# Optimization experiments

Measured on AMD Instinct MI355X. Metric: run time of the kernel, lower is better.

The kernel has to match this reference:

```python
import jax, jax.numpy as jnp
import numpy as np

H = 4096      # hidden_size
NH = 32       # num_heads
QR = 1536     # q_lora_rank
KVR = 512     # kv_lora_rank
RD = 64       # qk_rope_head_dim
ND = 128      # qk_nope_head_dim
VD = 128      # v_head_dim
QK = RD + ND  # qk_head_dim
EPS = 1e-6
THETA = 10000.0
B, S = 2, 1024


def rmsnorm(x, w):
    # torch: x / (||x|| * d^-0.5 + eps) * w
    norm = jnp.sqrt(jnp.sum(x * x, axis=-1, keepdims=True)) * (x.shape[-1] ** -0.5)
    return x / (norm + EPS) * w


def rope_cos_sin(seq_len):
    inv_freq = 1.0 / (THETA ** (jnp.arange(0, RD, 2, dtype=jnp.float32) / RD))
    t = jnp.arange(seq_len, dtype=jnp.float32)
    freqs = jnp.outer(t, inv_freq)              # [S, RD/2]
    emb = jnp.concatenate([freqs, freqs], -1)   # [S, RD]
    return jnp.cos(emb), jnpp_cos_sin_dummy() if False else jnp.sin(emb)


def rotate_half(x):
    x1, x2 = jnp.split(x, 2, axis=-1)
    return jnp.concatenate([-x2, x1], axis=-1)


def setup_inputs() -> dict:
    key = jax.random.key(0)
    ks = jax.random.split(key, 8)
    sc = 0.02
    return {
        "hidden_states": jax.random.normal(ks[0], (B, S, H), jnp.float32),
        "w_qa": jax.random.normal(ks[1], (H, QR), jnp.float32) * sc,
        "g_qa": jnp.ones((QR,), jnp.float32),
        "w_qb": jax.random.normal(ks[2], (QR, NH * QK), jnp.float32) * sc,
        "w_kva": jax.random.normal(ks[3], (H, KVR + RD), jnp.float32) * sc,
        "g_kva": jnp.ones((KVR,), jnp.float32),
        "w_kvb": jax.random.normal(ks[4], (KVR, NH * (ND + VD)), jnp.float32) * sc,
        "w_o": jax.random.normal(ks[5], (NH * VD, H), jnp.float32) * sc,
    }


def reference(hidden_states, w_qa, g_qa, w_qb, w_kva, g_kva, w_kvb, w_o):
    b, s, _ = hidden_states.shape
    # Q path: LoRA down -> RMSNorm -> LoRA up
    q_c = rmsnorm(hidden_states @ w_qa, g_qa)                       # [b,s,QR]
    q = (q_c @ w_qb).reshape(b, s, NH, QK).transpose(0, 2, 1, 3)    # [b,NH,s,QK]
    q_nope, q_rope = q[..., :ND], q[..., ND:]
    # KV path: joint down-proj, split compressed kv and rope key
    kv = hidden_states @ w_kva                                      # [b,s,KVR+RD]
    k_c, k_rope = kv[..., :KVR], kv[..., KVR:]
    k_c = rmsnorm(k_c, g_kva)
    kst = (k_c @ w_kvb).reshape(b, s, NH, ND + VD).transpose(0, 2, 1, 3)
    k_nope, v = kst[..., :ND], kst[..., ND:]                        # [b,NH,s,ND],[b,NH,s,VD]
    # partial RoPE on the rope slice only
    inv_freq = 1.0 / (THETA ** (jnp.arange(0, RD, 2, dtype=jnp.float32) / RD))
    freqs = jnp.outer(jnp.arange(s, dtype=jnp.float32), inv_freq)
    emb = jnp.concatenate([freqs, freqs], -1)                       # [s,RD]
    cos = jnp.cos(emb)[None, None]                                  # [1,1,s,RD]
    sin = jnp.sin(emb)[None, None]
    k_rope = k_rope[:, None]                                        # [b,1,s,RD]
    q_rope = q_rope * cos + rotate_half(q_rope) * sin
    k_rope = k_rope * cos + rotate_half(k_rope) * sin
    k_rope = jnp.broadcast_to(k_rope, (b, NH, s, RD))
    query = jnp.concatenate([q_nope, q_rope], -1)                   # [b,NH,s,QK]
    key_s = jnp.concatenate([k_nope, k_rope], -1)
    scaling = QK ** -0.5
    scores = jnp.einsum("bhqd,bhkd->bhqk", query, key_s) * scaling  # [b,NH,s,s]
    attn = jax.nn.softmax(scores, axis=-1)
    out = jnp.einsum("bhqk,bhkd->bhqd", attn, v)                    # [b,NH,s,VD]
    out = out.transpose(0, 2, 1, 3).reshape(b, s, NH * VD)
    return out @ w_o                                                # [b,s,H]
```

## Files before the change

### kernel.cpp

```cpp
#include <hip/hip_runtime.h>
#include <hip/hip_bf16.h>
#include <stdint.h>

typedef float f32x4_t __attribute__((ext_vector_type(4)));
typedef short s16x8_t __attribute__((ext_vector_type(8)));

#define LDS_AS __attribute__((address_space(3)))
#define GLB_AS __attribute__((address_space(1)))

__device__ __forceinline__ void gload16(void* lds, const void* g) {
    __builtin_amdgcn_global_load_lds((const GLB_AS uint32_t*)g,
                                     (LDS_AS uint32_t*)lds, 16, 0, 0);
}

__global__ __launch_bounds__(256) void rope_table_kernel(float* __restrict__ cos_t,
                                                         float* __restrict__ sin_t) {
    int idx = blockIdx.x * 256 + threadIdx.x;
    int s = idx >> 6, j = idx & 63;
    float invf = powf(10000.0f, -((float)((j & 31) * 2)) / 64.0f);
    float a = (float)s * invf;
    cos_t[idx] = cosf(a);
    sin_t[idx] = sinf(a);
}

__global__ __launch_bounds__(256) void f32_to_bf16_kernel(const float* __restrict__ in,
                                                          __hip_bfloat16* __restrict__ out, int n4) {
    int i = blockIdx.x * 256 + threadIdx.x;
    if (i >= n4) return;
    float4 v = reinterpret_cast<const float4*>(in)[i];
    struct __align__(8) BF4 { __hip_bfloat16 a, b, c, d; } r;
    r.a = __float2bfloat16(v.x); r.b = __float2bfloat16(v.y);
    r.c = __float2bfloat16(v.z); r.d = __float2bfloat16(v.w);
    reinterpret_cast<BF4*>(out)[i] = r;
}

__global__ __launch_bounds__(256) void transpose_convert(const float* __restrict__ W,
                                                         __hip_bfloat16* __restrict__ WT,
                                                         int K, int N, int Npad) {
    __shared__ float tile[32][33];
    int k0 = blockIdx.y * 32, n0 = blockIdx.x * 32;
    int tx = threadIdx.x & 31, ty = threadIdx.x >> 5;
#pragma unroll
    for (int i = 0; i < 4; i++) {
        int ky = i * 8 + ty;
        int n = n0 + tx;
        float v = 0.f;
        if (n < N) v = W[(size_t)(k0 + ky) * N + n];
        tile[ky][tx] = v;
    }
    __syncthreads();
#pragma unroll
    for (int i = 0; i < 4; i++) {
        int ny = i * 8 + ty;
        WT[(size_t)(n0 + ny) * K + k0 + tx] = __float2bfloat16(tile[tx][ny]);
    }
}

__global__ __launch_bounds__(256) void rmsnorm_kernel(const float* __restrict__ in,
                                                      const float* __restrict__ g,
                                                      __hip_bfloat16* __restrict__ out,
                                                      int cols, int in_stride) {
    int row = blockIdx.x;
    const float* x = in + (size_t)row * in_stride;
    float ss = 0.f;
    for (int c = threadIdx.x; c < cols; c += 256) { float v = x[c]; ss += v * v; }
#pragma unroll
    for (int off = 32; off > 0; off >>= 1) ss += __shfl_xor(ss, off);
    __shared__ float red[4];
    if ((threadIdx.x & 63) == 0) red[threadIdx.x >> 6] = ss;
    __syncthreads();
    float tot = red[0] + red[1] + red[2] + red[3];
    float rms = sqrtf(tot / (float)cols);
    float inv = 1.0f / (rms + 1e-6f);
    for (int c = threadIdx.x; c < cols; c += 256)
        out[(size_t)row * cols + c] = __float2bfloat16(x[c] * inv * g[c]);
}

__global__ __launch_bounds__(256) void rope_k_kernel(const float* __restrict__ kv,
                                                     const float* __restrict__ cos_t,
                                                     const float* __restrict__ sin_t,
                                                     __hip_bfloat16* __restrict__ k_rope) {
    int idx = blockIdx.x * 256 + threadIdx.x;
    int tok = idx >> 5, j = idx & 31;
    int s = tok & 1023;
    const float* x = kv + (size_t)tok * 640 + 512;
    float x1 = x[j], x2 = x[j + 32];
    float co = cos_t[s * 64 + j], si = sin_t[s * 64 + j];
    __hip_bfloat16* o = k_rope + (size_t)tok * 64;
    o[j]      = __float2bfloat16(x1 * co - x2 * si);
    o[j + 32] = __float2bfloat16(x2 * co + x1 * si);
}

__global__ __launch_bounds__(256) void rope_scale_q_kernel(__hip_bfloat16* __restrict__ q,
                                                           const float* __restrict__ cos_t,
                                                           const float* __restrict__ sin_t) {
    int tok = blockIdx.x;
    int s = tok & 1023;
    __hip_bfloat16* row = q + (size_t)tok * 6144;
    const float scale = 0.07216878364870323f;
    for (int i = threadIdx.x; i < 4096; i += 256) {
        int h = i >> 7, d = i & 127;
        int c = h * 192 + d;
        row[c] = __float2bfloat16(__bfloat162float(row[c]) * scale);
    }
    for (int i = threadIdx.x; i < 1024; i += 256) {
        int h = i >> 5, j = i & 31;
        int c = h * 192 + 128 + j;
        float x1 = __bfloat162float(row[c]), x2 = __bfloat162float(row[c + 32]);
        float co = cos_t[s * 64 + j], si = sin_t[s * 64 + j];
        row[c]      = __float2bfloat16((x1 * co - x2 * si) * scale);
        row[c + 32] = __float2bfloat16((x2 * co + x1 * si) * scale);
    }
}

__global__ __launch_bounds__(256) void transpose_v_kernel(const __hip_bfloat16* __restrict__ kst,
                                                          __hip_bfloat16* __restrict__ V_T) {
    __shared__ __hip_bfloat16 t[64][136];
    int bid = blockIdx.x;
    int st = bid & 15, bh = bid >> 4;
    int h = bh & 31, b = bh >> 5;
    int s0 = st * 64;
#pragma unroll
    for (int i = 0; i < 4; i++) {
        int c = i * 256 + threadIdx.x;
        int r = c >> 4, oct = c & 15;
        *(s16x8_t*)&t[r][oct * 8] =
            *(const s16x8_t*)&kst[(size_t)(b * 1024 + s0 + r) * 8192 + h * 256 + 128 + oct * 8];
    }
    __syncthreads();
#pragma unroll
    for (int i = 0; i < 4; i++) {
        int c = i * 256 + threadIdx.x;
        int vd = c >> 3, oct = c & 7;
        s16x8_t pk;
#pragma unroll
        for (int e = 0; e < 8; e++) pk[e] = *(const short*)&t[oct * 8 + e][vd];
        *(s16x8_t*)&V_T[((size_t)bh * 128 + vd) * 1024 + s0 + oct * 8] = pk;
    }
}

template <int OUT_BF16>
__global__ __launch_bounds__(256, 2) void gemm_bt_128(const __hip_bfloat16* __restrict__ A,
                                                      const __hip_bfloat16* __restrict__ BT,
                                                      void* __restrict__ Cout,
                                                      int M, int N, int K) {
    __shared__ __hip_bfloat16 As[128 * 64];
    __shared__ __hip_bfloat16 Bs[128 * 64];
    const int tid = threadIdx.x;
    const int l = tid & 63, w = tid >> 6;
    const int wr = w >> 1, wc = w & 1;
    const int m0 = blockIdx.y * 128, n0 = blockIdx.x * 128;
    const int lrow = l & 15, lkg = l >> 4;

    f32x4_t acc[4][4];
#pragma unroll
    for (int i = 0; i < 4; i++)
#pragma unroll
        for (int j = 0; j < 4; j++) acc[i][j] = (f32x4_t){0.f, 0.f, 0.f, 0.f};

    for (int k0 = 0; k0 < K; k0 += 64) {
        __syncthreads();
#pragma unroll
        for (int i = 0; i < 4; i++) {
            int s = i * 256 + tid;
            int row = s >> 3, po = s & 7;
            int lo = po ^ (row & 7);
            gload16(&As[s * 8], &A[(size_t)(m0 + row) * K + k0 + lo * 8]);
            gload16(&Bs[s * 8], &BT[(size_t)(n0 + row) * K + k0 + lo * 8]);
        }
        __syncthreads();
#pragma unroll
        for (int ks = 0; ks < 2; ks++) {
            s16x8_t a[4], b[4];
#pragma unroll
            for (int m = 0; m < 4; m++) {
                int row = wr * 64 + m * 16 + lrow;
                int oct = (ks * 4 + lkg) ^ (row & 7);
                a[m] = *(const s16x8_t*)&As[row * 64 + oct * 8];
            }
#pragma unroll
            for (int n = 0; n < 4; n++) {
                int row = wc * 64 + n * 16 + lrow;
                int oct = (ks * 4 + lkg) ^ (row & 7);
                b[n] = *(const s16x8_t*)&Bs[row * 64 + oct * 8];
            }
#pragma unroll
            for (int m = 0; m < 4; m++)
#pragma unroll
                for (int n = 0; n < 4; n++)
                    acc[m][n] = __builtin_amdgcn_mfma_f32_16x16x32_bf16(a[m], b[n], acc[m][n], 0, 0, 0);
        }
    }
#pragma unroll
    for (int m = 0; m < 4; m++) {
        int row = m0 + wr * 64 + m * 16 + lkg * 4;
#pragma unroll
        for (int n = 0; n < 4; n++) {
            int col = n0 + wc * 64 + n * 16 + lrow;
#pragma unroll
            for (int r = 0; r < 4; r++) {
                float v = acc[m][n][r];
                if (OUT_BF16)
                    ((__hip_bfloat16*)Cout)[(size_t)(row + r) * N + col] = __float2bfloat16(v);
                else
                    ((float*)Cout)[(size_t)(row + r) * N + col] = v;
            }
        }
    }
}

__global__ __launch_bounds__(256, 2) void attn2_kernel(const __hip_bfloat16* __restrict__ q,
                                                       const __hip_bfloat16* __restrict__ kst,
                                                       const __hip_bfloat16* __restrict__ k_rope,
                                                       const __hip_bfloat16* __restrict__ V_T,
                                                       __hip_bfloat16* __restrict__ attn_out) {
    __shared__ __align__(16) __hip_bfloat16 Ks[2][64 * 192];
    __shared__ __align__(16) __hip_bfloat16 Ps[64 * 72];

    int i = blockIdx.x;
    int bh = (i & 7) * 8 + ((i >> 3) & 7);
    int qt = i >> 6;
    int h = bh & 31, b = bh >> 5;
    int q0 = qt * 64;
    int tid = threadIdx.x, l = tid & 63, w = tid >> 6;
    int lrow = l & 15, lkg = l >> 4;

    s16x8_t qa[6];
    {
        size_t qbase = (size_t)(b * 1024 + q0 + w * 16 + lrow) * 6144 + h * 192;
#pragma unroll
        for (int f = 0; f < 6; f++)
            qa[f] = *(const s16x8_t*)&q[qbase + f * 32 + lkg * 8];
    }
    f32x4_t acc_o[8];
#pragma unroll
    for (int n = 0; n < 8; n++) acc_o[n] = (f32x4_t){0.f, 0.f, 0.f, 0.f};
    float m_run[4] = {-1e30f, -1e30f, -1e30f, -1e30f};
    float l_run[4] = {0.f, 0.f, 0.f, 0.f};

    size_t krow_base = (size_t)(b * 1024) * 8192 + h * 256;
    size_t rrow_base = (size_t)(b * 1024) * 64;

    auto stage_k = [&](int kv0, int buf) {
#pragma unroll
        for (int it = 0; it < 6; it++) {
            int s = it * 256 + tid;
            int row = s / 24, po = s - row * 24;
            int lo = po ^ (row & 7);
            const __hip_bfloat16* src = (lo < 16)
                ? &kst[krow_base + (size_t)(kv0 + row) * 8192 + lo * 8]
                : &k_rope[rrow_base + (size_t)(kv0 + row) * 64 + (lo - 16) * 8];
            gload16(&Ks[buf][s * 8], src);
        }
    };

    stage_k(0, 0);
    asm volatile("s_waitcnt vmcnt(0)" ::: "memory");
    __syncthreads();

    int cur = 0;
    for (int kt = 0; kt < 16; kt++) {
        int kv0 = kt * 64;
        if (kt < 15) stage_k(kv0 + 64, cur ^ 1);

        f32x4_t sc[4];
#pragma unroll
        for (int c = 0; c < 4; c++) sc[c] = (f32x4_t){0.f, 0.f, 0.f, 0.f};
        __builtin_amdgcn_s_setprio(1);
#pragma unroll
        for (int c = 0; c < 4; c++) {
            int row = c * 16 + lrow;
#pragma unroll
            for (int f = 0; f < 6; f++) {
                int po = ((f * 4 + lkg) ^ (lrow & 7)) * 8;
                s16x8_t kb = *(const s16x8_t*)&Ks[cur][row * 192 + po];
                sc[c] = __builtin_amdgcn_mfma_f32_16x16x32_bf16(qa[f], kb, sc[c], 0, 0, 0);
            }
        }
        __builtin_amdgcn_s_setprio(0);

        s16x8_t vb[2][8];
#pragma unroll
        for (int kk = 0; kk < 2; kk++)
#pragma unroll
            for (int n = 0; n < 8; n++)
                vb[kk][n] = *(const s16x8_t*)&V_T[((size_t)(bh * 128 + n * 16 + lrow)) * 1024 +
                                                  kv0 + kk * 32 + lkg * 8];

        float mx[4];
#pragma unroll
        for (int r = 0; r < 4; r++) {
            float m0 = fmaxf(fmaxf(sc[0][r], sc[1][r]), fmaxf(sc[2][r], sc[3][r]));
#pragma unroll
            for (int off = 1; off < 16; off <<= 1) m0 = fmaxf(m0, __shfl_xor(m0, off));
            mx[r] = m0;
        }
        int small = (mx[0] - m_run[0] <= 8.0f) && (mx[1] - m_run[1] <= 8.0f) &&
                    (mx[2] - m_run[2] <= 8.0f) && (mx[3] - m_run[3] <= 8.0f);
        if (!__all(small)) {
#pragma unroll
            for (int r = 0; r < 4; r++) {
                float mn = fmaxf(m_run[r], mx[r]);
                float al = __expf(m_run[r] - mn);
                m_run[r] = mn;
                l_run[r] *= al;
#pragma unroll
                for (int n = 0; n < 8; n++) acc_o[n][r] *= al;
            }
        }
        float p[4][4];
#pragma unroll
        for (int r = 0; r < 4; r++) {
            float sum = 0.f;
#pragma unroll
            for (int c = 0; c < 4; c++) {
                float pv = __expf(sc[c][r] - m_run[r]);
                p[c][r] = pv;
                sum += pv;
            }
#pragma unroll
            for (int off = 1; off < 16; off <<= 1) sum += __shfl_xor(sum, off);
            l_run[r] += sum;
        }

#pragma unroll
        for (int c = 0; c < 4; c++)
#pragma unroll
            for (int r = 0; r < 4; r++)
                Ps[(w * 16 + lkg * 4 + r) * 72 + c * 16 + lrow] = __float2bfloat16(p[c][r]);
        asm volatile("s_waitcnt lgkmcnt(0)" ::: "memory");
        __builtin_amdgcn_s_setprio(1);
#pragma unroll
        for (int kk = 0; kk < 2; kk++) {
            s16x8_t pa = *(const s16x8_t*)&Ps[(w * 16 + lrow) * 72 + kk * 32 + lkg * 8];
#pragma unroll
            for (int n = 0; n < 8; n++)
                acc_o[n] = __builtin_amdgcn_mfma_f32_16x16x32_bf16(pa, vb[kk][n], acc_o[n], 0, 0, 0);
        }
        __builtin_amdgcn_s_setprio(0);

        asm volatile("s_waitcnt vmcnt(0)" ::: "memory");
        __syncthreads();
        cur ^= 1;
    }
#pragma unroll
    for (int r = 0; r < 4; r++) {
        float inv = 1.0f / l_run[r];
        size_t tok = (size_t)(b * 1024 + q0 + w * 16 + lkg * 4 + r);
#pragma unroll
        for (int n = 0; n < 8; n++)
            attn_out[tok * 4096 + h * 128 + n * 16 + lrow] =
                __float2bfloat16(acc_o[n][r] * inv);
    }
}

extern "C" void kernel_launch(void* const* d_in, const int* in_sizes, int n_in,
                              void* d_out, int out_size, void* d_ws, size_t ws_size,
                              hipStream_t stream) {
    const float* hidden = (const float*)d_in[0];
    const float* w_qa   = (const float*)d_in[1];
    const float* g_qa   = (const float*)d_in[2];
    const float* w_qb   = (const float*)d_in[3];
    const float* w_kva  = (const float*)d_in[4];
    const float* g_kva  = (const float*)d_in[5];
    const float* w_kvb  = (const float*)d_in[6];
    const float* w_o    = (const float*)d_in[7];
    float* out = (float*)d_out;

    char* base = (char*)d_ws;
    size_t off = 0;
    auto alloc = [&](size_t bytes) -> void* {
        off = (off + 255) & ~(size_t)255;
        void* p = base + off;
        off += bytes;
        return p;
    };
    float* cos_t = (float*)alloc(1024 * 64 * 4);
    float* sin_t = (float*)alloc(1024 * 64 * 4);
    __hip_bfloat16* hid_b  = (__hip_bfloat16*)alloc(2048ull * 4096 * 2);
    __hip_bfloat16* wqaT   = (__hip_bfloat16*)alloc(1536ull * 4096 * 2);
    __hip_bfloat16* wqbT   = (__hip_bfloat16*)alloc(6144ull * 1536 * 2);
    __hip_bfloat16* wkvaT  = (__hip_bfloat16*)alloc(640ull * 4096 * 2);
    __hip_bfloat16* wkvbT  = (__hip_bfloat16*)alloc(8192ull * 512 * 2);
    __hip_bfloat16* woT    = (__hip_bfloat16*)alloc(4096ull * 4096 * 2);
    float* q_a             = (float*)alloc(2048ull * 1536 * 4);
    __hip_bfloat16* q_c    = (__hip_bfloat16*)alloc(2048ull * 1536 * 2);
    __hip_bfloat16* q_buf  = (__hip_bfloat16*)alloc(2048ull * 6144 * 2);
    float* kv              = (float*)alloc(2048ull * 640 * 4);
    __hip_bfloat16* k_c    = (__hip_bfloat16*)alloc(2048ull * 512 * 2);
    __hip_bfloat16* k_rope = (__hip_bfloat16*)alloc(2048ull * 64 * 2);
    __hip_bfloat16* kst    = (__hip_bfloat16*)alloc(2048ull * 8192 * 2);
    __hip_bfloat16* V_T      = hid_b;
    __hip_bfloat16* attn_out = wqbT;

    rope_table_kernel<<<256, 256, 0, stream>>>(cos_t, sin_t);
    f32_to_bf16_kernel<<<8192, 256, 0, stream>>>(hidden, hid_b, 2048 * 4096 / 4);
    transpose_convert<<<dim3(1536 / 32, 4096 / 32), 256, 0, stream>>>(w_qa, wqaT, 4096, 1536, 1536);
    transpose_convert<<<dim3(640 / 32, 4096 / 32), 256, 0, stream>>>(w_kva, wkvaT, 4096, 576, 640);
    transpose_convert<<<dim3(6144 / 32, 1536 / 32), 256, 0, stream>>>(w_qb, wqbT, 1536, 6144, 6144);
    transpose_convert<<<dim3(8192 / 32, 512 / 32), 256, 0, stream>>>(w_kvb, wkvbT, 512, 8192, 8192);
    transpose_convert<<<dim3(4096 / 32, 4096 / 32), 256, 0, stream>>>(w_o, woT, 4096, 4096, 4096);

    gemm_bt_128<0><<<dim3(1536 / 128, 16), 256, 0, stream>>>(hid_b, wqaT, q_a, 2048, 1536, 4096);
    gemm_bt_128<0><<<dim3(640 / 128, 16), 256, 0, stream>>>(hid_b, wkvaT, kv, 2048, 640, 4096);
    rmsnorm_kernel<<<2048, 256, 0, stream>>>(q_a, g_qa, q_c, 1536, 1536);
    rmsnorm_kernel<<<2048, 256, 0, stream>>>(kv, g_kva, k_c, 512, 640);
    rope_k_kernel<<<2048 * 32 / 256, 256, 0, stream>>>(kv, cos_t, sin_t, k_rope);
    gemm_bt_128<1><<<dim3(6144 / 128, 16), 256, 0, stream>>>(q_c, wqbT, q_buf, 2048, 6144, 1536);
    rope_scale_q_kernel<<<2048, 256, 0, stream>>>(q_buf, cos_t, sin_t);
    gemm_bt_128<1><<<dim3(8192 / 128, 16), 256, 0, stream>>>(k_c, wkvbT, kst, 2048, 8192, 512);
    transpose_v_kernel<<<1024, 256, 0, stream>>>(kst, V_T);
    attn2_kernel<<<1024, 256, 0, stream>>>(q_buf, kst, k_rope, V_T, attn_out);
    gemm_bt_128<0><<<dim3(4096 / 128, 16), 256, 0, stream>>>(attn_out, woT, out, 2048, 4096, 4096);
}
```

Before: 538.4 us.

## Fold q scaling into w_qb, widen attention to 128-row query tiles, prefetch V

The softmax scaling is folded into the transposed w_qb weights, so the q RoPE kernel no longer rescales the nope part and touches only the rope slice. The attention kernel now uses 512 threads over 128 query rows per block, halving the grid so each staged K tile serves twice as many queries. V fragment loads are issued before the QK^T MMAs so their latency overlaps compute. Risks include higher LDS and register pressure per block with 512 threads, and the qt indexing must stay consistent with the new grid.

Result: slower. 783.0 us (+45.4%).

```diff
diff --git a/kernel.cpp b/kernel.cpp
--- a/kernel.cpp
+++ b/kernel.cpp
@@ -36,7 +36,7 @@
 
 __global__ __launch_bounds__(256) void transpose_convert(const float* __restrict__ W,
                                                          __hip_bfloat16* __restrict__ WT,
-                                                         int K, int N, int Npad) {
+                                                         int K, int N, int Npad, float scale) {
     __shared__ float tile[32][33];
     int k0 = blockIdx.y * 32, n0 = blockIdx.x * 32;
     int tx = threadIdx.x & 31, ty = threadIdx.x >> 5;
@@ -52,7 +52,7 @@
 #pragma unroll
     for (int i = 0; i < 4; i++) {
         int ny = i * 8 + ty;
-        WT[(size_t)(n0 + ny) * K + k0 + tx] = __float2bfloat16(tile[tx][ny]);
+        WT[(size_t)(n0 + ny) * K + k0 + tx] = __float2bfloat16(tile[tx][ny] * scale);
     }
 }
 
@@ -91,25 +91,21 @@
     o[j + 32] = __float2bfloat16(x2 * co + x1 * si);
 }
 
-__global__ __launch_bounds__(256) void rope_scale_q_kernel(__hip_bfloat16* __restrict__ q,
-                                                           const float* __restrict__ cos_t,
-                                                           const float* __restrict__ sin_t) {
+__global__ __launch_bounds__(256) void rope_q_kernel(__hip_bfloat16* __restrict__ q,
+                                                     const float* __restrict__ cos_t,
+                                                     const float* __restrict__ sin_t) {
     int tok = blockIdx.x;
     int s = tok & 1023;
     __hip_bfloat16* row = q + (size_t)tok * 6144;
-    const float scale = 0.07216878364870323f;
-    for (int i = threadIdx.x; i < 4096; i += 256) {
-        int h = i >> 7, d = i & 127;
-        int c = h * 192 + d;
-        row[c] = __float2bfloat16(__bfloat162float(row[c]) * scale);
-    }
-    for (int i = threadIdx.x; i < 1024; i += 256) {
+#pragma unroll
+    for (int it = 0; it < 4; it++) {
+        int i = it * 256 + threadIdx.x;
         int h = i >> 5, j = i & 31;
         int c = h * 192 + 128 + j;
         float x1 = __bfloat162float(row[c]), x2 = __bfloat162float(row[c + 32]);
         float co = cos_t[s * 64 + j], si = sin_t[s * 64 + j];
-        row[c]      = __float2bfloat16((x1 * co - x2 * si) * scale);
-        row[c + 32] = __float2bfloat16((x2 * co + x1 * si) * scale);
+        row[c]      = __float2bfloat16(x1 * co - x2 * si);
+        row[c + 32] = __float2bfloat16(x2 * co + x1 * si);
     }
 }
 
@@ -209,19 +205,19 @@
     }
 }
 
-__global__ __launch_bounds__(256, 2) void attn2_kernel(const __hip_bfloat16* __restrict__ q,
+__global__ __launch_bounds__(512, 4) void attn3_kernel(const __hip_bfloat16* __restrict__ q,
                                                        const __hip_bfloat16* __restrict__ kst,
                                                        const __hip_bfloat16* __restrict__ k_rope,
                                                        const __hip_bfloat16* __restrict__ V_T,
                                                        __hip_bfloat16* __restrict__ attn_out) {
     __shared__ __align__(16) __hip_bfloat16 Ks[2][64 * 192];
-    __shared__ __align__(16) __hip_bfloat16 Ps[64 * 72];
+    __shared__ __align__(16) __hip_bfloat16 Ps[128 * 72];
 
     int i = blockIdx.x;
     int bh = (i & 7) * 8 + ((i >> 3) & 7);
     int qt = i >> 6;
     int h = bh & 31, b = bh >> 5;
-    int q0 = qt * 64;
+    int q0 = qt * 128;
     int tid = threadIdx.x, l = tid & 63, w = tid >> 6;
     int lrow = l & 15, lkg = l >> 4;
 
@@ -243,8 +239,8 @@
 
     auto stage_k = [&](int kv0, int buf) {
 #pragma unroll
-        for (int it = 0; it < 6; it++) {
-            int s = it * 256 + tid;
+        for (int it = 0; it < 3; it++) {
+            int s = it * 512 + tid;
             int row = s / 24, po = s - row * 24;
             int lo = po ^ (row & 7);
             const __hip_bfloat16* src = (lo < 16)
@@ -261,6 +257,15 @@
     int cur = 0;
     for (int kt = 0; kt < 16; kt++) {
         int kv0 = kt * 64;
+
+        s16x8_t vb[2][8];
+#pragma unroll
+        for (int kk = 0; kk < 2; kk++)
+#pragma unroll
+            for (int n = 0; n < 8; n++)
+                vb[kk][n] = *(const s16x8_t*)&V_T[((size_t)(bh * 128 + n * 16 + lrow)) * 1024 +
+                                                  kv0 + kk * 32 + lkg * 8];
+
         if (kt < 15) stage_k(kv0 + 64, cur ^ 1);
 
         f32x4_t sc[4];
@@ -278,14 +283,6 @@
             }
         }
         __builtin_amdgcn_s_setprio(0);
-
-        s16x8_t vb[2][8];
-#pragma unroll
-        for (int kk = 0; kk < 2; kk++)
-#pragma unroll
-            for (int n = 0; n < 8; n++)
-                vb[kk][n] = *(const s16x8_t*)&V_T[((size_t)(bh * 128 + n * 16 + lrow)) * 1024 +
-                                                  kv0 + kk * 32 + lkg * 8];
 
         float mx[4];
 #pragma unroll
@@ -393,13 +390,15 @@
     __hip_bfloat16* V_T      = hid_b;
     __hip_bfloat16* attn_out = wqbT;
 
+    const float qscale = 0.07216878364870323f;
+
     rope_table_kernel<<<256, 256, 0, stream>>>(cos_t, sin_t);
     f32_to_bf16_kernel<<<8192, 256, 0, stream>>>(hidden, hid_b, 2048 * 4096 / 4);
-    transpose_convert<<<dim3(1536 / 32, 4096 / 32), 256, 0, stream>>>(w_qa, wqaT, 4096, 1536, 1536);
-    transpose_convert<<<dim3(640 / 32, 4096 / 32), 256, 0, stream>>>(w_kva, wkvaT, 4096, 576, 640);
-    transpose_convert<<<dim3(6144 / 32, 1536 / 32), 256, 0, stream>>>(w_qb, wqbT, 1536, 6144, 6144);
-    transpose_convert<<<dim3(8192 / 32, 512 / 32), 256, 0, stream>>>(w_kvb, wkvbT, 512, 8192, 8192);
-    transpose_convert<<<dim3(4096 / 32, 4096 / 32), 256, 0, stream>>>(w_o, woT, 4096, 4096, 4096);
+    transpose_convert<<<dim3(1536 / 32, 4096 / 32), 256, 0, stream>>>(w_qa, wqaT, 4096, 1536, 1536, 1.0f);
+    transpose_convert<<<dim3(640 / 32, 4096 / 32), 256, 0, stream>>>(w_kva, wkvaT, 4096, 576, 640, 1.0f);
+    transpose_convert<<<dim3(6144 / 32, 1536 / 32), 256, 0, stream>>>(w_qb, wqbT, 1536, 6144, 6144, qscale);
+    transpose_convert<<<dim3(8192 / 32, 512 / 32), 256, 0, stream>>>(w_kvb, wkvbT, 512, 8192, 8192, 1.0f);
+    transpose_convert<<<dim3(4096 / 32, 4096 / 32), 256, 0, stream>>>(w_o, woT, 4096, 4096, 4096, 1.0f);
 
     gemm_bt_128<0><<<dim3(1536 / 128, 16), 256, 0, stream>>>(hid_b, wqaT, q_a, 2048, 1536, 4096);
     gemm_bt_128<0><<<dim3(640 / 128, 16), 256, 0, stream>>>(hid_b, wkvaT, kv, 2048, 640, 4096);
@@ -407,9 +406,9 @@
     rmsnorm_kernel<<<2048, 256, 0, stream>>>(kv, g_kva, k_c, 512, 640);
     rope_k_kernel<<<2048 * 32 / 256, 256, 0, stream>>>(kv, cos_t, sin_t, k_rope);
     gemm_bt_128<1><<<dim3(6144 / 128, 16), 256, 0, stream>>>(q_c, wqbT, q_buf, 2048, 6144, 1536);
-    rope_scale_q_kernel<<<2048, 256, 0, stream>>>(q_buf, cos_t, sin_t);
+    rope_q_kernel<<<2048, 256, 0, stream>>>(q_buf, cos_t, sin_t);
     gemm_bt_128<1><<<dim3(8192 / 128, 16), 256, 0, stream>>>(k_c, wkvbT, kst, 2048, 8192, 512);
     transpose_v_kernel<<<1024, 256, 0, stream>>>(kst, V_T);
-    attn2_kernel<<<1024, 256, 0, stream>>>(q_buf, kst, k_rope, V_T, attn_out);
+    attn3_kernel<<<512, 512, 0, stream>>>(q_buf, kst, k_rope, V_T, attn_out);
     gemm_bt_128<0><<<dim3(4096 / 128, 16), 256, 0, stream>>>(attn_out, woT, out, 2048, 4096, 4096);
 }
```
